# Performance work log

Measured on AMD Instinct MI355X. Metric: run time of the kernel, lower is better.

## Reference

```python
import jax, jax.numpy as jnp
import numpy as np

VOCAB = 50257
HIDDEN = [1024, 512]
NUM_CLASSES = 20


def setup_inputs() -> dict:
    key = jax.random.key(0)
    ks = jax.random.split(key, 8)
    B, S = 1024, 512
    x = jax.random.randint(ks[0], (B, S), 0, VOCAB, dtype=jnp.int32)
    def lin(kw, kb, fan_in, fan_out):
        lim = 1.0 / np.sqrt(fan_in)
        W = jax.random.uniform(kw, (fan_in, fan_out), minval=-lim, maxval=lim, dtype=jnp.float32)
        b = jax.random.uniform(kb, (fan_out,), minval=-lim, maxval=lim, dtype=jnp.float32)
        return W, b
    W1, b1 = lin(ks[1], ks[2], VOCAB, HIDDEN[0])
    W2, b2 = lin(ks[3], ks[4], HIDDEN[0], HIDDEN[1])
    Wout, bout = lin(ks[5], ks[6], HIDDEN[1], NUM_CLASSES)
    return {"x": x, "W1": W1, "b1": b1, "W2": W2, "b2": b2, "Wout": Wout, "bout": bout}


def bow_counts(x, vocab):
    # Fused batched histogram: scatter-add of ones into a flat [B*V] buffer.
    B = x.shape[0]
    flat = (jnp.arange(B, dtype=x.dtype)[:, None] * vocab + x).reshape(-1)
    bow = jnp.zeros((B * vocab,), dtype=jnp.float32).at[flat].add(1.0)
    return bow.reshape(B, vocab)


def reference(x, W1, b1, W2, b2, Wout, bout):
    bow = bow_counts(x, VOCAB)                       # [B, V]
    h = jax.nn.relu(bow @ W1 + b1)                   # [B, 1024]
    h = jax.nn.relu(h @ W2 + b2)                     # [B, 512]  (dropout = identity at inference)
    return h @ Wout + bout                           # [B, num_classes]
```

## Files before the change

kernel.cpp:

```cpp
#include <hip/hip_runtime.h>

#define VOCAB 50257
#define BATCH 1024
#define SEQ   512
#define H1    1024
#define H2    512
#define NC    20

typedef float floatx4 __attribute__((ext_vector_type(4)));

#define NRANGE 128
#define RNGW   393
#define NSTEP  (NRANGE / 8)
#define RPB    4
#define TPB    (RPB * SEQ)
#define NRT    (BATCH / RPB)
#define FLATCAP 448
#define SENT   (RPB << 16)

__global__ __launch_bounds__(256) void k1_range(
    const int* __restrict__ x, const float* __restrict__ W1,
    float* __restrict__ px) {
    const int b   = blockIdx.x;
    const int xcd = b & 7;
    const int rt  = b >> 3;
    const int r0  = rt * RPB;
    const int tid = threadIdx.x;

    __shared__ int toks[TPB];
    __shared__ int flat[FLATCAP];
    __shared__ int cnt[NSTEP], pref[NSTEP], fill[NSTEP];
    __shared__ int tot_s;

    if (tid < NSTEP) { cnt[tid] = 0; fill[tid] = 0; }
    __syncthreads();

#pragma unroll
    for (int k = 0; k < TPB / 256; ++k) {
        const int j = k * 256 + tid;
        const int t = __builtin_nontemporal_load(&x[(size_t)r0 * SEQ + j]);
        toks[j] = t;
        const int rng = t / RNGW;
        if ((rng & 7) == xcd) atomicAdd(&cnt[rng >> 3], 1);
    }
    __syncthreads();

    if (tid == 0) {
        int s = 0;
#pragma unroll
        for (int i = 0; i < NSTEP; ++i) { pref[i] = s; s += cnt[i]; }
        tot_s = s;
    }
    __syncthreads();

#pragma unroll
    for (int k = 0; k < TPB / 256; ++k) {
        const int j = k * 256 + tid;
        const int t = toks[j];
        const int rng = t / RNGW;
        if ((rng & 7) == xcd) {
            const int pos = pref[rng >> 3] + atomicAdd(&fill[rng >> 3], 1);
            if (pos < FLATCAP) flat[pos] = ((j >> 9) << 16) | t;
        }
    }
    __syncthreads();
    {
        const int tot  = tot_s;
        const int npad = (tot + 7) & ~7;
        if (tid < npad - tot) flat[tot + tid] = SENT;
    }
    __syncthreads();

    floatx4 a0 = (floatx4)0.f, a1 = (floatx4)0.f,
            a2 = (floatx4)0.f, a3 = (floatx4)0.f;

#define RFL(v)  __builtin_amdgcn_readfirstlane(v)
#define LDW(e)  (*((const floatx4*)(W1 + (size_t)((e) & 0xFFFF) * H1) + tid))
#define ACC(e, w)                                                            \
    do {                                                                     \
        switch ((e) >> 16) {                                                 \
            case 0: a0 += (w); break;                                        \
            case 1: a1 += (w); break;                                        \
            case 2: a2 += (w); break;                                        \
            case 3: a3 += (w); break;                                        \
            default: break;                                                  \
        }                                                                    \
    } while (0)

    const int ntot = RFL((tot_s + 7) & ~7);
    if (ntot > 0) {
        const int ng = ntot >> 3;
        const int* lp = flat;

        int e0 = RFL(lp[0]), e1 = RFL(lp[1]), e2 = RFL(lp[2]), e3 = RFL(lp[3]),
            e4 = RFL(lp[4]), e5 = RFL(lp[5]), e6 = RFL(lp[6]), e7 = RFL(lp[7]);
        floatx4 w0 = LDW(e0), w1 = LDW(e1), w2 = LDW(e2), w3 = LDW(e3),
                w4 = LDW(e4), w5 = LDW(e5), w6 = LDW(e6), w7 = LDW(e7);

        for (int g = 0; g + 1 < ng; ++g) {
            const int* lq = lp + (g + 1) * 8;
            const int f0 = RFL(lq[0]), f1 = RFL(lq[1]), f2 = RFL(lq[2]),
                      f3 = RFL(lq[3]), f4 = RFL(lq[4]), f5 = RFL(lq[5]),
                      f6 = RFL(lq[6]), f7 = RFL(lq[7]);
            const floatx4 v0 = LDW(f0), v1 = LDW(f1), v2 = LDW(f2),
                          v3 = LDW(f3), v4 = LDW(f4), v5 = LDW(f5),
                          v6 = LDW(f6), v7 = LDW(f7);
            ACC(e0, w0); ACC(e1, w1); ACC(e2, w2); ACC(e3, w3);
            ACC(e4, w4); ACC(e5, w5); ACC(e6, w6); ACC(e7, w7);
            e0 = f0; e1 = f1; e2 = f2; e3 = f3;
            e4 = f4; e5 = f5; e6 = f6; e7 = f7;
            w0 = v0; w1 = v1; w2 = v2; w3 = v3;
            w4 = v4; w5 = v5; w6 = v6; w7 = v7;
        }
        ACC(e0, w0); ACC(e1, w1); ACC(e2, w2); ACC(e3, w3);
        ACC(e4, w4); ACC(e5, w5); ACC(e6, w6); ACC(e7, w7);
    }
#undef ACC
#undef LDW
#undef RFL

    floatx4* dst = (floatx4*)(px + ((size_t)xcd * BATCH + r0) * H1) + tid;
    __builtin_nontemporal_store(a0, dst + 0 * (H1 / 4));
    __builtin_nontemporal_store(a1, dst + 1 * (H1 / 4));
    __builtin_nontemporal_store(a2, dst + 2 * (H1 / 4));
    __builtin_nontemporal_store(a3, dst + 3 * (H1 / 4));
}

__global__ __launch_bounds__(256) void k1b_reduce(
    const float* __restrict__ px, float* __restrict__ p) {
    const size_t i4 = (size_t)blockIdx.x * 256 + threadIdx.x;
    const floatx4* s = (const floatx4*)px + i4;
    floatx4 a = __builtin_nontemporal_load(s);
#pragma unroll
    for (int xc = 1; xc < 8; ++xc)
        a += __builtin_nontemporal_load(s + (size_t)xc * BATCH * (H1 / 4));
    ((floatx4*)p)[i4] = a;
}

template<int SSPLIT>
__global__ __launch_bounds__(256) void k1_gather(
    const int* __restrict__ x, const float* __restrict__ W1,
    float* __restrict__ p) {
    const int row = blockIdx.x / SSPLIT;
    const int s   = blockIdx.x % SSPLIT;
    const int tid = threadIdx.x;
    constexpr int TOK = SEQ / SSPLIT;

    __shared__ int toks[TOK];
    for (int i = tid; i < TOK; i += 256) toks[i] = x[row * SEQ + s * TOK + i];
    __syncthreads();

    floatx4 acc = (floatx4)0.f;
#pragma unroll 8
    for (int t = 0; t < TOK; ++t)
        acc += ((const floatx4*)(W1 + (size_t)toks[t] * H1))[tid];
    ((floatx4*)p)[((size_t)s * BATCH + row) * (H1 / 4) + tid] = acc;
}

template<int NPART>
__global__ __launch_bounds__(256) void k2_gemm(
    const float* __restrict__ p, const float* __restrict__ b1,
    const float* __restrict__ W2, const float* __restrict__ b2,
    float* __restrict__ h2) {
    __shared__ float As[16][H1];
    const int tid = threadIdx.x;
    const int rt  = blockIdx.x >> 2;
    const int ct  = blockIdx.x & 3;
    const int r0  = rt * 16;

    const float* __restrict__ p1 = p + (size_t)BATCH * H1;

    for (int i = tid; i < 16 * (H1 / 4); i += 256) {
        const int r  = i >> 8;
        const int k4 = i & 255;
        float4 v = ((const float4*)(p + ((size_t)(r0 + r)) * H1))[k4];
        if (NPART == 2) {
            const float4 u = ((const float4*)(p1 + ((size_t)(r0 + r)) * H1))[k4];
            v.x += u.x; v.y += u.y; v.z += u.z; v.w += u.w;
        }
        const float4 bb = ((const float4*)b1)[k4];
        As[r][k4 * 4 + 0] = fmaxf(v.x + bb.x, 0.f);
        As[r][k4 * 4 + 1] = fmaxf(v.y + bb.y, 0.f);
        As[r][k4 * 4 + 2] = fmaxf(v.z + bb.z, 0.f);
        As[r][k4 * 4 + 3] = fmaxf(v.w + bb.w, 0.f);
    }
    __syncthreads();

    const int q  = tid & 31;
    const int ks = tid >> 5;

    float4 acc[16];
#pragma unroll
    for (int r = 0; r < 16; ++r) acc[r] = make_float4(0.f, 0.f, 0.f, 0.f);

    const float* __restrict__ w2base = W2 + (size_t)ct * 128 + q * 4;
#pragma unroll 2
    for (int kk = 0; kk < 128; ++kk) {
        const int k = ks * 128 + kk;
        const float4 w = *(const float4*)(w2base + (size_t)k * H2);
#pragma unroll
        for (int r = 0; r < 16; ++r) {
            const float a = As[r][k];
            acc[r].x += a * w.x; acc[r].y += a * w.y;
            acc[r].z += a * w.z; acc[r].w += a * w.w;
        }
    }

    __syncthreads();
    float4* Rs = (float4*)As;
#define RS(rs, r) Rs[(((rs) * 32 + q) * 16) + (r)]
    if (ks >= 4) {
#pragma unroll
        for (int r = 0; r < 16; ++r) RS(ks - 4, r) = acc[r];
    }
    __syncthreads();
    if (ks < 4) {
#pragma unroll
        for (int r = 0; r < 16; ++r) {
            const float4 t = RS(ks, r);
            acc[r].x += t.x; acc[r].y += t.y; acc[r].z += t.z; acc[r].w += t.w;
        }
    }
    __syncthreads();
    if (ks == 2 || ks == 3) {
#pragma unroll
        for (int r = 0; r < 16; ++r) RS(ks - 2, r) = acc[r];
    }
    __syncthreads();
    if (ks < 2) {
#pragma unroll
        for (int r = 0; r < 16; ++r) {
            const float4 t = RS(ks, r);
            acc[r].x += t.x; acc[r].y += t.y; acc[r].z += t.z; acc[r].w += t.w;
        }
    }
    __syncthreads();
    if (ks == 1) {
#pragma unroll
        for (int r = 0; r < 16; ++r) RS(0, r) = acc[r];
    }
    __syncthreads();
    if (ks == 0) {
        const float4 bb = *(const float4*)(b2 + ct * 128 + q * 4);
#pragma unroll
        for (int r = 0; r < 16; ++r) {
            const float4 t = RS(0, r);
            float4 o;
            o.x = fmaxf(acc[r].x + t.x + bb.x, 0.f);
            o.y = fmaxf(acc[r].y + t.y + bb.y, 0.f);
            o.z = fmaxf(acc[r].z + t.z + bb.z, 0.f);
            o.w = fmaxf(acc[r].w + t.w + bb.w, 0.f);
            *(float4*)(h2 + (size_t)(r0 + r) * H2 + ct * 128 + q * 4) = o;
        }
    }
#undef RS
}

__global__ __launch_bounds__(256) void k3_out(
    const float* __restrict__ h2, const float* __restrict__ Wout,
    const float* __restrict__ bout, float* __restrict__ out) {
    const int gid = blockIdx.x * 256 + threadIdx.x;
    const int r = gid >> 5;
    const int c = gid & 31;
    if (c >= NC) return;

    float acc = bout[c];
    const float* __restrict__ hrow = h2 + (size_t)r * H2;
#pragma unroll 8
    for (int k = 0; k < H2; ++k)
        acc += hrow[k] * Wout[k * NC + c];
    out[r * NC + c] = acc;
}

extern "C" void kernel_launch(void* const* d_in, const int* in_sizes, int n_in,
                              void* d_out, int out_size, void* d_ws, size_t ws_size,
                              hipStream_t stream) {
    const int*   x    = (const int*)d_in[0];
    const float* W1   = (const float*)d_in[1];
    const float* b1   = (const float*)d_in[2];
    const float* W2   = (const float*)d_in[3];
    const float* b2   = (const float*)d_in[4];
    const float* Wout = (const float*)d_in[5];
    const float* bout = (const float*)d_in[6];
    float* out = (float*)d_out;

    const size_t needA = ((size_t)8 * BATCH * H1 + (size_t)BATCH * H1 +
                          (size_t)BATCH * H2) * 4;
    const size_t need2 = ((size_t)2 * BATCH * H1 + (size_t)BATCH * H2) * 4;

    if (ws_size >= needA) {
        float* px = (float*)d_ws;
        float* p  = px + (size_t)8 * BATCH * H1;
        float* h2 = p + (size_t)BATCH * H1;
        k1_range<<<8 * NRT, 256, 0, stream>>>(x, W1, px);
        k1b_reduce<<<BATCH * H1 / 4 / 256, 256, 0, stream>>>(px, p);
        k2_gemm<1><<<256, 256, 0, stream>>>(p, b1, W2, b2, h2);
        k3_out<<<BATCH * 32 / 256, 256, 0, stream>>>(h2, Wout, bout, out);
    } else if (ws_size >= need2) {
        float* p  = (float*)d_ws;
        float* h2 = p + (size_t)2 * BATCH * H1;
        k1_gather<2><<<BATCH * 2, 256, 0, stream>>>(x, W1, p);
        k2_gemm<2><<<256, 256, 0, stream>>>(p, b1, W2, b2, h2);
        k3_out<<<BATCH * 32 / 256, 256, 0, stream>>>(h2, Wout, bout, out);
    } else {
        float* p  = (float*)d_ws;
        float* h2 = p + (size_t)BATCH * H1;
        k1_gather<1><<<BATCH, 256, 0, stream>>>(x, W1, p);
        k2_gemm<1><<<256, 256, 0, stream>>>(p, b1, W2, b2, h2);
        k3_out<<<BATCH * 32 / 256, 256, 0, stream>>>(h2, Wout, bout, out);
    }
}
```

Before: 277.1 us.

## Convert W1 to fp16 each call and gather with eight rows per block

A new conversion kernel turns the full fp32 W1 into an fp16 copy in workspace on every call. The range-partitioned gather kernel is templated on weight type and reads fp16 rows, halving the bytes moved per gathered row. Rows per block rise from 4 to 8, with matching flat-list capacity and accumulator count, so each loaded weight row serves more batch rows. The cost is an extra full pass over W1 (read fp32, write fp16) on every call, plus fp16 rounding of the weights.

```diff
diff --git a/kernel.cpp b/kernel.cpp
--- a/kernel.cpp
+++ b/kernel.cpp
@@ -7,28 +7,65 @@
 #define H2    512
 #define NC    20
 
-typedef float floatx4 __attribute__((ext_vector_type(4)));
+typedef float    floatx4 __attribute__((ext_vector_type(4)));
+typedef _Float16 halfx4  __attribute__((ext_vector_type(4)));
+typedef _Float16 halfx8  __attribute__((ext_vector_type(8)));
 
 #define NRANGE 128
 #define RNGW   393
 #define NSTEP  (NRANGE / 8)
-#define RPB    4
+#define RPB    8
 #define TPB    (RPB * SEQ)
 #define NRT    (BATCH / RPB)
-#define FLATCAP 448
+#define FLATCAP 768
+#define CAPP   (FLATCAP + 8)
 #define SENT   (RPB << 16)
 
-__global__ __launch_bounds__(256) void k1_range(
-    const int* __restrict__ x, const float* __restrict__ W1,
+template<typename T> struct VecT;
+template<> struct VecT<float>    { typedef floatx4 type; };
+template<> struct VecT<_Float16> { typedef halfx4  type; };
+
+__device__ __forceinline__ floatx4 toF4(floatx4 v) { return v; }
+__device__ __forceinline__ floatx4 toF4(halfx4 v) {
+    floatx4 r;
+    r[0] = (float)v[0]; r[1] = (float)v[1];
+    r[2] = (float)v[2]; r[3] = (float)v[3];
+    return r;
+}
+
+__global__ __launch_bounds__(256) void k0_conv(
+    const float* __restrict__ W1, _Float16* __restrict__ W1h) {
+    const size_t n8 = (size_t)VOCAB * H1 / 8;
+    const size_t stride = (size_t)gridDim.x * 256;
+    for (size_t j = (size_t)blockIdx.x * 256 + threadIdx.x; j < n8; j += stride) {
+        const floatx4 a =
+            __builtin_nontemporal_load((const floatx4*)W1 + 2 * j);
+        const floatx4 b =
+            __builtin_nontemporal_load((const floatx4*)W1 + 2 * j + 1);
+        halfx8 o;
+        o[0] = (_Float16)a[0]; o[1] = (_Float16)a[1];
+        o[2] = (_Float16)a[2]; o[3] = (_Float16)a[3];
+        o[4] = (_Float16)b[0]; o[5] = (_Float16)b[1];
+        o[6] = (_Float16)b[2]; o[7] = (_Float16)b[3];
+        __builtin_nontemporal_store(o, (halfx8*)W1h + j);
+    }
+}
+
+template<typename T>
+__global__ __launch_bounds__(256) void k1_rangeT(
+    const int* __restrict__ x, const T* __restrict__ Wt,
     float* __restrict__ px) {
+    using VT = typename VecT<T>::type;
     const int b   = blockIdx.x;
     const int xcd = b & 7;
     const int rt  = b >> 3;
     const int r0  = rt * RPB;
     const int tid = threadIdx.x;
+    const int li  = tid & 127;
+    const int cb  = (tid >> 7) * 512 + li * 4;
 
     __shared__ int toks[TPB];
-    __shared__ int flat[FLATCAP];
+    __shared__ int flat[CAPP];
     __shared__ int cnt[NSTEP], pref[NSTEP], fill[NSTEP];
     __shared__ int tot_s;
 
@@ -64,47 +101,49 @@
         }
     }
     __syncthreads();
-    {
-        const int tot  = tot_s;
-        const int npad = (tot + 7) & ~7;
-        if (tid < npad - tot) flat[tot + tid] = SENT;
-    }
-    __syncthreads();
-
-    floatx4 a0 = (floatx4)0.f, a1 = (floatx4)0.f,
-            a2 = (floatx4)0.f, a3 = (floatx4)0.f;
+    const int tot  = min(tot_s, FLATCAP);
+    const int npad = (tot + 7) & ~7;
+    if (tid < npad - tot) flat[tot + tid] = SENT;
+    __syncthreads();
+
+    floatx4 a0 = (floatx4)0.f, a1 = (floatx4)0.f, a2 = (floatx4)0.f,
+            a3 = (floatx4)0.f, a4 = (floatx4)0.f, a5 = (floatx4)0.f,
+            a6 = (floatx4)0.f, a7 = (floatx4)0.f;
+
+    const T* __restrict__ Wc = Wt + cb;
 
 #define RFL(v)  __builtin_amdgcn_readfirstlane(v)
-#define LDW(e)  (*((const floatx4*)(W1 + (size_t)((e) & 0xFFFF) * H1) + tid))
+#define LDW(e)  (*(const VT*)(Wc + (size_t)((e) & 0xFFFF) * H1))
 #define ACC(e, w)                                                            \
     do {                                                                     \
         switch ((e) >> 16) {                                                 \
-            case 0: a0 += (w); break;                                        \
-            case 1: a1 += (w); break;                                        \
-            case 2: a2 += (w); break;                                        \
-            case 3: a3 += (w); break;                                        \
+            case 0: a0 += toF4(w); break;                                    \
+            case 1: a1 += toF4(w); break;                                    \
+            case 2: a2 += toF4(w); break;                                    \
+            case 3: a3 += toF4(w); break;                                    \
+            case 4: a4 += toF4(w); break;                                    \
+            case 5: a5 += toF4(w); break;                                    \
+            case 6: a6 += toF4(w); break;                                    \
+            case 7: a7 += toF4(w); break;                                    \
             default: break;                                                  \
         }                                                                    \
     } while (0)
 
-    const int ntot = RFL((tot_s + 7) & ~7);
-    if (ntot > 0) {
-        const int ng = ntot >> 3;
+    const int ng = npad >> 3;
+    if (ng > 0) {
         const int* lp = flat;
-
         int e0 = RFL(lp[0]), e1 = RFL(lp[1]), e2 = RFL(lp[2]), e3 = RFL(lp[3]),
             e4 = RFL(lp[4]), e5 = RFL(lp[5]), e6 = RFL(lp[6]), e7 = RFL(lp[7]);
-        floatx4 w0 = LDW(e0), w1 = LDW(e1), w2 = LDW(e2), w3 = LDW(e3),
-                w4 = LDW(e4), w5 = LDW(e5), w6 = LDW(e6), w7 = LDW(e7);
+        VT w0 = LDW(e0), w1 = LDW(e1), w2 = LDW(e2), w3 = LDW(e3),
+           w4 = LDW(e4), w5 = LDW(e5), w6 = LDW(e6), w7 = LDW(e7);
 
         for (int g = 0; g + 1 < ng; ++g) {
             const int* lq = lp + (g + 1) * 8;
             const int f0 = RFL(lq[0]), f1 = RFL(lq[1]), f2 = RFL(lq[2]),
                       f3 = RFL(lq[3]), f4 = RFL(lq[4]), f5 = RFL(lq[5]),
                       f6 = RFL(lq[6]), f7 = RFL(lq[7]);
-            const floatx4 v0 = LDW(f0), v1 = LDW(f1), v2 = LDW(f2),
-                          v3 = LDW(f3), v4 = LDW(f4), v5 = LDW(f5),
-                          v6 = LDW(f6), v7 = LDW(f7);
+            const VT v0 = LDW(f0), v1 = LDW(f1), v2 = LDW(f2), v3 = LDW(f3),
+                     v4 = LDW(f4), v5 = LDW(f5), v6 = LDW(f6), v7 = LDW(f7);
             ACC(e0, w0); ACC(e1, w1); ACC(e2, w2); ACC(e3, w3);
             ACC(e4, w4); ACC(e5, w5); ACC(e6, w6); ACC(e7, w7);
             e0 = f0; e1 = f1; e2 = f2; e3 = f3;
@@ -119,11 +158,15 @@
 #undef LDW
 #undef RFL
 
-    floatx4* dst = (floatx4*)(px + ((size_t)xcd * BATCH + r0) * H1) + tid;
-    __builtin_nontemporal_store(a0, dst + 0 * (H1 / 4));
-    __builtin_nontemporal_store(a1, dst + 1 * (H1 / 4));
-    __builtin_nontemporal_store(a2, dst + 2 * (H1 / 4));
-    __builtin_nontemporal_store(a3, dst + 3 * (H1 / 4));
+    float* pb = px + ((size_t)xcd * BATCH + r0) * H1 + cb;
+    __builtin_nontemporal_store(a0, (floatx4*)(pb + 0 * H1));
+    __builtin_nontemporal_store(a1, (floatx4*)(pb + 1 * H1));
+    __builtin_nontemporal_store(a2, (floatx4*)(pb + 2 * H1));
+    __builtin_nontemporal_store(a3, (floatx4*)(pb + 3 * H1));
+    __builtin_nontemporal_store(a4, (floatx4*)(pb + 4 * H1));
+    __builtin_nontemporal_store(a5, (floatx4*)(pb + 5 * H1));
+    __builtin_nontemporal_store(a6, (floatx4*)(pb + 6 * H1));
+    __builtin_nontemporal_store(a7, (floatx4*)(pb + 7 * H1));
 }
 
 __global__ __launch_bounds__(256) void k1b_reduce(
@@ -284,19 +327,30 @@
     const float* bout = (const float*)d_in[6];
     float* out = (float*)d_out;
 
-    const size_t needA = ((size_t)8 * BATCH * H1 + (size_t)BATCH * H1 +
-                          (size_t)BATCH * H2) * 4;
-    const size_t need2 = ((size_t)2 * BATCH * H1 + (size_t)BATCH * H2) * 4;
-
-    if (ws_size >= needA) {
+    const size_t W1HB = (size_t)VOCAB * H1 * 2;
+    const size_t PXB  = (size_t)8 * BATCH * H1 * 4;
+    const size_t PB   = (size_t)BATCH * H1 * 4;
+    const size_t H2BB = (size_t)BATCH * H2 * 4;
+
+    if (ws_size >= W1HB + PXB + PB + H2BB) {
+        _Float16* W1h = (_Float16*)d_ws;
+        float* px = (float*)((char*)d_ws + W1HB);
+        float* p  = px + (size_t)8 * BATCH * H1;
+        float* h2 = p + (size_t)BATCH * H1;
+        k0_conv<<<4096, 256, 0, stream>>>(W1, W1h);
+        k1_rangeT<_Float16><<<8 * NRT, 256, 0, stream>>>(x, W1h, px);
+        k1b_reduce<<<BATCH * H1 / 4 / 256, 256, 0, stream>>>(px, p);
+        k2_gemm<1><<<256, 256, 0, stream>>>(p, b1, W2, b2, h2);
+        k3_out<<<BATCH * 32 / 256, 256, 0, stream>>>(h2, Wout, bout, out);
+    } else if (ws_size >= PXB + PB + H2BB) {
         float* px = (float*)d_ws;
         float* p  = px + (size_t)8 * BATCH * H1;
         float* h2 = p + (size_t)BATCH * H1;
-        k1_range<<<8 * NRT, 256, 0, stream>>>(x, W1, px);
+        k1_rangeT<float><<<8 * NRT, 256, 0, stream>>>(x, W1, px);
         k1b_reduce<<<BATCH * H1 / 4 / 256, 256, 0, stream>>>(px, p);
         k2_gemm<1><<<256, 256, 0, stream>>>(p, b1, W2, b2, h2);
         k3_out<<<BATCH * 32 / 256, 256, 0, stream>>>(h2, Wout, bout, out);
-    } else if (ws_size >= need2) {
+    } else if (ws_size >= (size_t)2 * BATCH * H1 * 4 + H2BB) {
         float* p  = (float*)d_ws;
         float* h2 = p + (size_t)2 * BATCH * H1;
         k1_gather<2><<<BATCH * 2, 256, 0, stream>>>(x, W1, p);
```

New measurement: 244.7 us. -11.7%, faster.
